# Kernel tuning notes

Measured on AMD Instinct MI355X. Metric: run time of the kernel, lower is better.

## Reference

```python
import jax, jax.numpy as jnp
import numpy as np

TOP_K = 2          # routed top_k = top_k - num_shared_experts = 3 - 1
CAP_FACTOR = 1.1   # capacity_factor


def setup_inputs() -> dict:
    key = jax.random.key(0)
    ks = jax.random.split(key, 12)
    B, S, D, E = 4, 2048, 1024, 7
    s = 0.02
    return {
        "x": jax.random.normal(ks[0], (B, S, D), jnp.float32),
        "noise": jax.random.normal(ks[1], (B, S, E), jnp.float32),
        "Wr": jax.random.normal(ks[2], (D, E)) * s, "br": jnp.zeros((E,)),
        "Wn": jax.random.normal(ks[3], (D, E)) * s, "bn": jnp.zeros((E,)),
        "W1": jax.random.normal(ks[4], (E, D, D)) * s, "b1": jnp.zeros((E, D)),
        "W2": jax.random.normal(ks[5], (E, D, D)) * s, "b2": jnp.zeros((E, D)),
        "Ws1": jax.random.normal(ks[6], (D, D)) * s, "bs1": jnp.zeros((D,)),
        "Ws2": jax.random.normal(ks[7], (D, D)) * s, "bs2": jnp.zeros((D,)),
    }


def reference(x, noise, Wr, br, Wn, bn, W1, b1, W2, b2, Ws1, bs1, Ws2, bs2):
    B, S, D = x.shape
    E = Wr.shape[1]
    N = B * S
    C = int(N * TOP_K / E * CAP_FACTOR)  # per-expert capacity (static)

    # shared expert (Dropout inactive at inference)
    x_shared = jax.nn.relu(x @ Ws1 + bs1) @ Ws2 + bs2

    # --- noisy top-k router ---
    logits = x @ Wr + br
    noisy = logits + noise * jax.nn.softplus(x @ Wn + bn)
    vals, idx = jax.lax.top_k(noisy, TOP_K)                    # [B,S,K]
    onehot = jax.nn.one_hot(idx, E, dtype=x.dtype)             # [B,S,K,E]
    probs_k = jax.nn.softmax(vals, axis=-1)                    # softmax over -inf-masked logits == softmax over top-k vals
    router_probs = jnp.einsum('bske,bsk->bse', onehot, probs_k)
    expert_mask = onehot.sum(-2)
    lbl = E * (router_probs.mean((0, 1)) * expert_mask.mean((0, 1))).sum()

    # --- capacity-limited dispatch, first-come-first-served in flat token order ---
    flat_x = x.reshape(N, D)
    flat_g = router_probs.reshape(N, E)
    m = (expert_mask.reshape(N, E) > 0).T                      # [E,N] token->expert assignment
    pos = jnp.cumsum(m.astype(jnp.int32), axis=1) - 1          # slot within expert
    valid = m & (pos < C)
    token = jnp.arange(N, dtype=jnp.int32)
    dest = jnp.where(valid, jnp.arange(E, dtype=jnp.int32)[:, None] * C + pos, E * C)
    idxs = jnp.full((E * C + 1,), N, dtype=jnp.int32)
    idxs = idxs.at[dest.reshape(-1)].set(jnp.broadcast_to(token, (E, N)).reshape(-1))
    idxs = idxs[:E * C].reshape(E, C)                          # token id per slot, N = padding

    xpad = jnp.concatenate([flat_x, jnp.zeros((1, D), x.dtype)], axis=0)
    gpad = jnp.concatenate([flat_g, jnp.zeros((1, E), x.dtype)], axis=0)
    xe = xpad[idxs]                                            # [E,C,D]
    h = jax.nn.relu(jnp.einsum('ecd,edh->ech', xe, W1) + b1[:, None, :])
    out = jnp.einsum('ech,ehd->ecd', h, W2) + b2[:, None, :]
    g = (gpad[idxs] * jnp.eye(E, dtype=x.dtype)[:, None, :]).sum(-1)  # [E,C] gate per slot
    slot_valid = (idxs < N).astype(x.dtype)
    weighted = out * (g * slot_valid)[..., None]

    upd = jnp.zeros((N + 1, D), x.dtype).at[idxs.reshape(-1)].add(weighted.reshape(-1, D))[:N]
    final = upd.reshape(B, S, D) + x_shared
    return final, lbl
```

## Files before the change

kernel.cpp:

```cpp
#include <hip/hip_runtime.h>
#include <math.h>

typedef unsigned short u16;
typedef __attribute__((ext_vector_type(4))) float f32x4;
typedef __bf16 bf16x8 __attribute__((ext_vector_type(8)));

#define NTOK 8192
#define DDIM 1024
#define NEXP 7
#define CAPC 2574
#define CPAD 2688
#define MBE8 11
#define EB8 (NEXP * MBE8 * 4)
#define TB8 (EB8 + 32 * 4)

__device__ inline float bf2f(u16 u) {
    union { unsigned int i; float f; } c; c.i = ((unsigned int)u) << 16; return c.f;
}
__device__ inline u16 f2bf(float f) {
    union { float f; unsigned int i; } c; c.f = f;
    unsigned int u = c.i;
    unsigned int r = (u + 0x7fffu + ((u >> 16) & 1u)) >> 16;
    return (u16)r;
}

__device__ inline void gl2lds16(const u16* g, const u16* l) {
    __builtin_amdgcn_global_load_lds(
        (const __attribute__((address_space(1))) unsigned int*)g,
        (__attribute__((address_space(3))) unsigned int*)l, 16, 0, 0);
}

#define BAR()    asm volatile("s_barrier" ::: "memory")
#define WAITV0() asm volatile("s_waitcnt vmcnt(0)" ::: "memory")

__global__ void k_zero(float* out, long n) {
    long i = (long)blockIdx.x * 256 + threadIdx.x;
    long stride = (long)gridDim.x * 256;
    for (; i < n; i += stride) out[i] = 0.f;
}

__global__ void k_prep(const float* __restrict__ x, u16* __restrict__ xb,
                       int* __restrict__ slot_token, u16* __restrict__ zrow,
                       const float* __restrict__ W1, const float* __restrict__ Ws1,
                       u16* __restrict__ Wt, u16* __restrict__ Wst,
                       const float* __restrict__ W2, const float* __restrict__ Ws2,
                       u16* __restrict__ Wt2, u16* __restrict__ Wst2) {
    int bid = blockIdx.x, tid = threadIdx.x;
    if (bid < 4096) {
        int gid = bid * 256 + tid;
        int i = gid * 8;
        float4 a = *(const float4*)(x + i);
        float4 b = *(const float4*)(x + i + 4);
        ushort4 o0; o0.x = f2bf(a.x); o0.y = f2bf(a.y); o0.z = f2bf(a.z); o0.w = f2bf(a.w);
        ushort4 o1; o1.x = f2bf(b.x); o1.y = f2bf(b.y); o1.z = f2bf(b.z); o1.w = f2bf(b.w);
        *(ushort4*)(xb + i) = o0;
        *(ushort4*)(xb + i + 4) = o1;
        if (gid < DDIM) zrow[gid] = 0;
        if (gid < NEXP * CPAD + 128) slot_token[gid] = NTOK;
        return;
    }
    int phase2 = (bid >= 8192);
    int tb = bid - (phase2 ? 8192 : 4096);
    const float* srcE = phase2 ? W2 : W1;
    const float* srcS = phase2 ? Ws2 : Ws1;
    u16* dE = phase2 ? Wt2 : Wt;
    u16* dS = phase2 ? Wst2 : Wst;
    int z = tb >> 9; int rem = tb & 511;
    int y = rem >> 2; int xq = rem & 3;
    const float* src; u16* dst;
    if (z < 7) { src = srcE + (long)z * 1048576; dst = dE + (long)z * 1048576; }
    else       { src = srcS;                     dst = dS; }
    int n = xq * 256 + tid;
    int k0 = y * 8;
    u16 v[8];
#pragma unroll
    for (int j = 0; j < 8; ++j) v[j] = f2bf(src[(long)(k0 + j) * 1024 + n]);
    ushort4 a; a.x = v[0]; a.y = v[1]; a.z = v[2]; a.w = v[3];
    ushort4 b; b.x = v[4]; b.y = v[5]; b.z = v[6]; b.w = v[7];
    *(ushort4*)(dst + (long)n * 1024 + k0) = a;
    *(ushort4*)(dst + (long)n * 1024 + k0 + 4) = b;
}

__global__ void k_transpose(const float* __restrict__ srcE, const float* __restrict__ srcS,
                            u16* __restrict__ Wt, u16* __restrict__ Wst) {
    int z = blockIdx.z;
    const float* src; u16* dst;
    if (z < 7) { src = srcE + (long)z * 1048576; dst = Wt + (long)z * 1048576; }
    else       { src = srcS;                     dst = Wst; }
    int n = blockIdx.x * 256 + threadIdx.x;
    int k0 = blockIdx.y * 8;
    u16 v[8];
#pragma unroll
    for (int j = 0; j < 8; ++j) v[j] = f2bf(src[(long)(k0 + j) * 1024 + n]);
    ushort4 a; a.x = v[0]; a.y = v[1]; a.z = v[2]; a.w = v[3];
    ushort4 b; b.x = v[4]; b.y = v[5]; b.z = v[6]; b.w = v[7];
    *(ushort4*)(dst + (long)n * 1024 + k0) = a;
    *(ushort4*)(dst + (long)n * 1024 + k0 + 4) = b;
}

__global__ __launch_bounds__(512) void k_router(
    const float* __restrict__ x,
    const float* __restrict__ Wr, const float* __restrict__ Wn,
    double* __restrict__ arO, double* __restrict__ anO) {
    __shared__ float swr[7168];
    __shared__ float swn[7168];
    int tid = threadIdx.x;
    for (int i = tid; i < 7168; i += 512) { swr[i] = Wr[i]; swn[i] = Wn[i]; }
    __syncthreads();
    int lane = tid & 63, wv = tid >> 6;
    int t = blockIdx.x * 8 + wv;
    double ar[7] = {0,0,0,0,0,0,0}, an[7] = {0,0,0,0,0,0,0};
    for (int j = 0; j < 16; ++j) {
        int d = j * 64 + lane;
        double xd = (double)x[t * 1024 + d];
#pragma unroll
        for (int e = 0; e < 7; ++e) {
            ar[e] += xd * (double)swr[d * 7 + e];
            an[e] += xd * (double)swn[d * 7 + e];
        }
    }
#pragma unroll
    for (int e = 0; e < 7; ++e) {
        for (int o = 32; o > 0; o >>= 1) {
            ar[e] += __shfl_xor(ar[e], o);
            an[e] += __shfl_xor(an[e], o);
        }
    }
    if (lane == 0) {
#pragma unroll
        for (int e = 0; e < 7; ++e) { arO[t * 7 + e] = ar[e]; anO[t * 7 + e] = an[e]; }
    }
}

__global__ void k_tail(const double* __restrict__ arO, const double* __restrict__ anO,
                       const float* __restrict__ noise,
                       const float* __restrict__ br, const float* __restrict__ bn,
                       int* __restrict__ idx0, int* __restrict__ idx1,
                       float* __restrict__ p0, float* __restrict__ p1,
                       int* __restrict__ cntA, double* __restrict__ sumA) {
    int t = blockIdx.x * 256 + threadIdx.x;
    int lane = threadIdx.x & 63;
    double best = -1e300, second = -1e300; int b0 = 0, b1 = 0;
#pragma unroll
    for (int e = 0; e < 7; ++e) {
        double lg = arO[t * 7 + e] + (double)br[e];
        double z  = anO[t * 7 + e] + (double)bn[e];
        double sp = (z > 30.0) ? (z + log1p(exp(-z))) : log1p(exp(z));
        double v  = lg + (double)noise[t * 7 + e] * sp;
        if (v > best)        { second = best; b1 = b0; best = v; b0 = e; }
        else if (v > second) { second = v; b1 = e; }
    }
    double ex = exp(second - best);
    float q0 = (float)(1.0 / (1.0 + ex));
    float q1 = (float)(ex / (1.0 + ex));
    idx0[t] = b0; idx1[t] = b1; p0[t] = q0; p1[t] = q1;
    int chunk = t >> 6;
    double dq0 = (double)q0, dq1 = (double)q1;
#pragma unroll
    for (int e = 0; e < 7; ++e) {
        unsigned long long m = __ballot((b0 == e) || (b1 == e));
        double q = (b0 == e ? dq0 : 0.0) + (b1 == e ? dq1 : 0.0);
        for (int o = 32; o > 0; o >>= 1) q += __shfl_xor(q, o);
        if (lane == 0) { cntA[e * 128 + chunk] = __popcll(m); sumA[e * 128 + chunk] = q; }
    }
}

__global__ void k_scanbase(const int* __restrict__ cntA, const double* __restrict__ sumA,
                           int* __restrict__ baseA, int* __restrict__ cnt,
                           float* __restrict__ out) {
    __shared__ int s[128];
    __shared__ double rd[128];
    __shared__ int rawc[7];
    __shared__ double ps[7];
    int tid = threadIdx.x;
    for (int e = 0; e < 7; ++e) {
        int v = 0;
        if (tid < 128) { v = cntA[e * 128 + tid]; s[tid] = v; }
        if (tid < 128) rd[tid] = sumA[e * 128 + tid];
        __syncthreads();
        for (int o = 1; o < 128; o <<= 1) {
            int add = 0;
            if (tid < 128 && tid >= o) add = s[tid - o];
            __syncthreads();
            if (tid < 128) s[tid] += add;
            __syncthreads();
        }
        if (tid < 128) baseA[e * 128 + tid] = s[tid] - v;
        if (tid == 127) { rawc[e] = s[127]; cnt[e] = (s[127] < CAPC) ? s[127] : CAPC; }
        for (int o = 64; o > 0; o >>= 1) {
            if (tid < o) rd[tid] += rd[tid + o];
            __syncthreads();
        }
        if (tid == 0) ps[e] = rd[0];
        __syncthreads();
    }
    if (tid == 0) {
        double acc = 0.0;
        for (int e = 0; e < 7; ++e) acc += ps[e] * (double)rawc[e];
        out[(long)NTOK * DDIM] = (float)(7.0 * acc / (8192.0 * 8192.0));
    }
}

__global__ void k_assign(const int* __restrict__ idx0, const int* __restrict__ idx1,
                         const int* __restrict__ baseA, int* __restrict__ slot_token,
                         int* __restrict__ ts0, int* __restrict__ ts1) {
    int lane = threadIdx.x & 63;
    int chunk = (blockIdx.x * 256 + threadIdx.x) >> 6;
    int t = chunk * 64 + lane;
    int i0 = idx0[t], i1 = idx1[t];
    int myts0 = -1, myts1 = -1;
    unsigned long long lt = (1ull << lane) - 1ull;
#pragma unroll
    for (int e = 0; e < 7; ++e) {
        bool has = (i0 == e) || (i1 == e);
        unsigned long long m = __ballot(has);
        int pre = __popcll(m & lt);
        int pos = baseA[e * 128 + chunk] + pre;
        if (has && pos < CAPC) {
            int slot = e * CPAD + pos;
            slot_token[slot] = t;
            if (i0 == e) myts0 = slot; else myts1 = slot;
        }
    }
    ts0[t] = myts0; ts1[t] = myts1;
}


#define READ_A(MQ)                                                                      \
    _Pragma("unroll")                                                                   \
    for (int j = 0; j < 4; ++j) {                                                       \
        int row_ = wm * 128 + (MQ) * 64 + j * 16 + rl;                                  \
        _Pragma("unroll")                                                               \
        for (int kh = 0; kh < 2; ++kh)                                                  \
            af[j][kh] = *(const bf16x8*)&sA[row_ * 64 + (((kh * 4 + quad) ^ kq7)) * 8]; \
    }

#define READ_B(NQ)                                                                      \
    _Pragma("unroll")                                                                   \
    for (int j = 0; j < 2; ++j) {                                                       \
        int row_ = wn * 64 + (NQ) * 32 + j * 16 + rl;                                   \
        _Pragma("unroll")                                                               \
        for (int kh = 0; kh < 2; ++kh)                                                  \
            bf[j][kh] = *(const bf16x8*)&sB[row_ * 64 + (((kh * 4 + quad) ^ kq7)) * 8]; \
    }

#define MFMA_Q(MQ, NQ)                                                                  \
    _Pragma("unroll")                                                                   \
    for (int kh = 0; kh < 2; ++kh)                                                      \
        _Pragma("unroll")                                                               \
        for (int j = 0; j < 4; ++j)                                                     \
            _Pragma("unroll")                                                           \
            for (int i = 0; i < 2; ++i)                                                 \
                acc[(MQ) * 4 + j][(NQ) * 2 + i] =                                       \
                    __builtin_amdgcn_mfma_f32_16x16x32_bf16(                            \
                        af[j][kh], bf[i][kh], acc[(MQ) * 4 + j][(NQ) * 2 + i], 0, 0, 0);

template <bool GATHER, bool MODE_H>
__global__ __launch_bounds__(512, 2) void k_gemm8(
    const u16* __restrict__ AbaseE, const u16* __restrict__ AbaseS,
    const int* __restrict__ gidx, const u16* __restrict__ zrow,
    const u16* __restrict__ WtE, const u16* __restrict__ WtS,
    const float* __restrict__ biasE, const float* __restrict__ biasS,
    u16* __restrict__ outE, u16* __restrict__ outS,
    const int* __restrict__ cnt) {
    extern __shared__ __align__(16) u16 lds[];
    int bid = blockIdx.x;
    int tid = threadIdx.x, lane = tid & 63, wv = tid >> 6;
    int lrow = lane >> 3, lkg = lane & 7, kgs = lkg ^ lrow;

    int e = 0, my, nx, mbound;
    const u16* Ab; const u16* Bb; const float* bias; u16* outp;
    bool gather = false;
    if (bid < EB8) {
        e = bid / 44; int r = bid % 44; my = r >> 2; nx = r & 3;
        if (my * 256 >= cnt[e]) return;
        Ab = GATHER ? AbaseE : (AbaseE + (long)e * CPAD * 1024);
        Bb = WtE + ((long)e << 20);
        bias = biasE + e * 1024;
        outp = outE + (long)e * CPAD * 1024;
        gather = GATHER;
        mbound = CPAD;
    } else {
        int sb = bid - EB8; my = sb >> 2; nx = sb & 3;
        Ab = AbaseS; Bb = WtS; bias = biasS; outp = outS;
        mbound = NTOK;
    }
    int m0 = my * 256, n0 = nx * 256;

    const u16* arow[4];
    const u16* brow[4];
#pragma unroll
    for (int i = 0; i < 4; ++i) {
        int r = (wv * 4 + i) * 8 + lrow;
        if (gather) {
            int tok = gidx[e * CPAD + m0 + r];
            arow[i] = (tok < NTOK) ? (AbaseE + (long)tok * DDIM) : zrow;
        } else {
            int rr = m0 + r; if (rr >= mbound) rr = 0;
            arow[i] = Ab + (long)rr * DDIM;
        }
        brow[i] = Bb + (long)(n0 + r) * DDIM;
    }

    f32x4 acc[8][4];
#pragma unroll
    for (int a = 0; a < 8; ++a)
#pragma unroll
        for (int b = 0; b < 4; ++b) { f32x4 z = {0.f, 0.f, 0.f, 0.f}; acc[a][b] = z; }

    int rl = lane & 15, quad = lane >> 4, kq7 = rl & 7;
    int wm = wv >> 2, wn = wv & 3;
    u16* s0 = lds;
    u16* s1 = lds + 32768;

#pragma unroll
    for (int i = 0; i < 4; ++i) {
        gl2lds16(arow[i] + kgs * 8, s0 + (wv * 4 + i) * 512);
        gl2lds16(brow[i] + kgs * 8, s0 + 16384 + (wv * 4 + i) * 512);
    }
    WAITV0();
    BAR();

    bf16x8 af[4][2], bf[2][2];
    for (int T = 0; T < 16; ++T) {
        u16* sc = (T & 1) ? s1 : s0;
        u16* sn = (T & 1) ? s0 : s1;
        const u16* sA = sc;
        const u16* sB = sc + 16384;
        int k1 = (T + 1) * 64;
        READ_A(0)
        READ_B(0)
        if (T < 15) {
#pragma unroll
            for (int i = 0; i < 4; ++i)
                gl2lds16(arow[i] + k1 + kgs * 8, sn + (wv * 4 + i) * 512);
        }
        BAR();
        __builtin_amdgcn_s_setprio(1);
        MFMA_Q(0, 0)
        __builtin_amdgcn_s_setprio(0);
        BAR();
        READ_B(1)
        if (T < 15) {
#pragma unroll
            for (int i = 0; i < 4; ++i)
                gl2lds16(brow[i] + k1 + kgs * 8, sn + 16384 + (wv * 4 + i) * 512);
        }
        BAR();
        __builtin_amdgcn_s_setprio(1);
        MFMA_Q(0, 1)
        __builtin_amdgcn_s_setprio(0);
        BAR();
        READ_A(1)
        BAR();
        __builtin_amdgcn_s_setprio(1);
        MFMA_Q(1, 1)
        __builtin_amdgcn_s_setprio(0);
        BAR();
        READ_B(0)
        BAR();
        __builtin_amdgcn_s_setprio(1);
        MFMA_Q(1, 0)
        __builtin_amdgcn_s_setprio(0);
        WAITV0();
        BAR();
        __builtin_amdgcn_sched_barrier(0);
    }

#pragma unroll
    for (int ni = 0; ni < 4; ++ni) {
        int col = n0 + wn * 64 + ni * 16 + rl;
        float bv = bias[col];
#pragma unroll
        for (int mi = 0; mi < 8; ++mi) {
            int rowb = m0 + wm * 128 + mi * 16 + quad * 4;
#pragma unroll
            for (int r = 0; r < 4; ++r) {
                int rowg = rowb + r;
                if (rowg < mbound) {
                    float v = acc[mi][ni][r] + bv;
                    if constexpr (MODE_H) v = v > 0.f ? v : 0.f;
                    outp[(long)rowg * DDIM + col] = f2bf(v);
                }
            }
        }
    }
}

__global__ __launch_bounds__(256) void k_combine(
    const u16* __restrict__ Xs, const u16* __restrict__ OutE,
    const int* __restrict__ ts0, const int* __restrict__ ts1,
    const float* __restrict__ p0, const float* __restrict__ p1,
    float* __restrict__ out) {
    int b = blockIdx.x;
    int d = threadIdx.x * 4;
    long base = (long)b * DDIM + d;
    ushort4 xs4 = *(const ushort4*)(Xs + base);
    float r0 = bf2f(xs4.x), r1 = bf2f(xs4.y), r2 = bf2f(xs4.z), r3 = bf2f(xs4.w);
    int s0 = ts0[b], s1 = ts1[b];
    if (s0 >= 0) {
        float g = p0[b];
        ushort4 o4 = *(const ushort4*)(OutE + (long)s0 * DDIM + d);
        r0 += g * bf2f(o4.x); r1 += g * bf2f(o4.y); r2 += g * bf2f(o4.z); r3 += g * bf2f(o4.w);
    }
    if (s1 >= 0) {
        float g = p1[b];
        ushort4 o4 = *(const ushort4*)(OutE + (long)s1 * DDIM + d);
        r0 += g * bf2f(o4.x); r1 += g * bf2f(o4.y); r2 += g * bf2f(o4.z); r3 += g * bf2f(o4.w);
    }
    float4 w; w.x = r0; w.y = r1; w.z = r2; w.w = r3;
    *(float4*)(out + base) = w;
}

extern "C" void kernel_launch(void* const* d_in, const int* in_sizes, int n_in,
                              void* d_out, int out_size, void* d_ws, size_t ws_size,
                              hipStream_t stream) {
    const float* x    = (const float*)d_in[0];
    const float* noise= (const float*)d_in[1];
    const float* Wr   = (const float*)d_in[2];
    const float* br   = (const float*)d_in[3];
    const float* Wn   = (const float*)d_in[4];
    const float* bn   = (const float*)d_in[5];
    const float* W1   = (const float*)d_in[6];
    const float* b1   = (const float*)d_in[7];
    const float* W2   = (const float*)d_in[8];
    const float* b2   = (const float*)d_in[9];
    const float* Ws1  = (const float*)d_in[10];
    const float* bs1  = (const float*)d_in[11];
    const float* Ws2  = (const float*)d_in[12];
    const float* bs2  = (const float*)d_in[13];
    float* out = (float*)d_out;
    char* ws = (char*)d_ws;

    size_t off = 0;
    auto alloc = [&](size_t bytes) { size_t o = off; off += (bytes + 255) & ~(size_t)255; return o; };
    u16*  Wt   = (u16*)(ws + alloc(7ull * 1048576 * 2));
    u16*  Wst  = (u16*)(ws + alloc(1048576ull * 2));
    u16*  xb   = (u16*)(ws + alloc((size_t)NTOK * 1024 * 2));
    u16*  He   = (u16*)(ws + alloc((size_t)NEXP * CPAD * 1024 * 2));
    u16*  Hs   = (u16*)(ws + alloc((size_t)NTOK * 1024 * 2));
    u16*  OutE = (u16*)(ws + alloc((size_t)NEXP * CPAD * 1024 * 2));
    u16*  Xs   = (u16*)(ws + alloc((size_t)NTOK * 1024 * 2));
    int*  idx0 = (int*)(ws + alloc(NTOK * 4));
    int*  idx1 = (int*)(ws + alloc(NTOK * 4));
    float* p0  = (float*)(ws + alloc(NTOK * 4));
    float* p1  = (float*)(ws + alloc(NTOK * 4));
    int*  ts0  = (int*)(ws + alloc(NTOK * 4));
    int*  ts1  = (int*)(ws + alloc(NTOK * 4));
    int*  slot_token = (int*)(ws + alloc((NEXP * CPAD + 128) * 4));
    int*  cntA = (int*)(ws + alloc(7 * 128 * 4));
    int*  baseA= (int*)(ws + alloc(7 * 128 * 4));
    double* sumA = (double*)(ws + alloc(7 * 128 * 8));
    int*  cnt    = (int*)(ws + alloc(8 * 4));
    u16*  zrow   = (u16*)(ws + alloc(1024 * 2));
    double* arO  = (double*)(ws + alloc((size_t)NTOK * 7 * 8));
    double* anO  = (double*)(ws + alloc((size_t)NTOK * 7 * 8));
    size_t base_off = off;
    u16*  Wt2  = (u16*)(ws + alloc(7ull * 1048576 * 2));
    u16*  Wst2 = (u16*)(ws + alloc(1048576ull * 2));

    if (base_off > ws_size) {
        k_zero<<<2048, 256, 0, stream>>>(out, (long)out_size);
        return;
    }
    bool sep = (off <= ws_size);
    if (!sep) { Wt2 = Wt; Wst2 = Wst; }

    (void)hipFuncSetAttribute((const void*)k_gemm8<true, true>,
                              hipFuncAttributeMaxDynamicSharedMemorySize, 131072);
    (void)hipFuncSetAttribute((const void*)k_gemm8<false, false>,
                              hipFuncAttributeMaxDynamicSharedMemorySize, 131072);

    k_prep<<<sep ? 12288 : 8192, 256, 0, stream>>>(
        x, xb, slot_token, zrow, W1, Ws1, Wt, Wst, W2, Ws2, Wt2, Wst2);
    k_router<<<1024, 512, 0, stream>>>(x, Wr, Wn, arO, anO);
    k_tail<<<32, 256, 0, stream>>>(arO, anO, noise, br, bn, idx0, idx1, p0, p1, cntA, sumA);
    k_scanbase<<<1, 256, 0, stream>>>(cntA, sumA, baseA, cnt, out);
    k_assign<<<32, 256, 0, stream>>>(idx0, idx1, baseA, slot_token, ts0, ts1);

    k_gemm8<true, true><<<TB8, 512, 131072, stream>>>(
        xb, xb, slot_token, zrow, Wt, Wst, b1, bs1, He, Hs, cnt);

    if (!sep)
        k_transpose<<<dim3(4, 128, 8), 256, 0, stream>>>(W2, Ws2, Wt, Wst);

    k_gemm8<false, false><<<TB8, 512, 131072, stream>>>(
        He, Hs, nullptr, zrow, Wt2, Wst2, b2, bs2, OutE, Xs, cnt);

    k_combine<<<NTOK, 256, 0, stream>>>(Xs, OutE, ts0, ts1, p0, p1, out);
    (void)in_sizes; (void)n_in; (void)out_size;
}
```

Measured before the change: 435.2 us.

## Pipeline GEMM with per-quadrant LDS staging, partial vmcnt waits and XCD-aware block swizzle

Restructures the MoE/shared GEMM main loop into an unrolled two-buffer ping-pong. Each A/B quadrant is staged into LDS separately and earlier than before, and partial vmcnt waits replace full drains, so global loads overlap more of the MFMA work. Block IDs are also remapped so that consecutive logical tiles, which share weight or activation panels, land on the same XCD to improve L2 reuse. The price is more complex buffer reuse logic, where a wrong wait count or overwrite order would race. The 2688 CPAD rows are also read without the old row clamp.

```diff
diff --git a/kernel.cpp b/kernel.cpp
--- a/kernel.cpp
+++ b/kernel.cpp
@@ -10,9 +10,10 @@
 #define NEXP 7
 #define CAPC 2574
 #define CPAD 2688
-#define MBE8 11
-#define EB8 (NEXP * MBE8 * 4)
+#define EB8 (NEXP * 11 * 4)
 #define TB8 (EB8 + 32 * 4)
+#define SWZQ (TB8 / 8)
+#define SWZR (TB8 % 8)
 
 __device__ inline float bf2f(u16 u) {
     union { unsigned int i; float f; } c; c.i = ((unsigned int)u) << 16; return c.f;
@@ -32,6 +33,8 @@
 
 #define BAR()    asm volatile("s_barrier" ::: "memory")
 #define WAITV0() asm volatile("s_waitcnt vmcnt(0)" ::: "memory")
+#define WAITV4() asm volatile("s_waitcnt vmcnt(4)" ::: "memory")
+#define WAITV6() asm volatile("s_waitcnt vmcnt(6)" ::: "memory")
 
 __global__ void k_zero(float* out, long n) {
     long i = (long)blockIdx.x * 256 + threadIdx.x;
@@ -226,25 +229,27 @@
 }
 
 
-#define READ_A(MQ)                                                                      \
+#define RD_AF(DST, MQ, BUF)                                                             \
     _Pragma("unroll")                                                                   \
     for (int j = 0; j < 4; ++j) {                                                       \
         int row_ = wm * 128 + (MQ) * 64 + j * 16 + rl;                                  \
         _Pragma("unroll")                                                               \
         for (int kh = 0; kh < 2; ++kh)                                                  \
-            af[j][kh] = *(const bf16x8*)&sA[row_ * 64 + (((kh * 4 + quad) ^ kq7)) * 8]; \
-    }
-
-#define READ_B(NQ)                                                                      \
+            DST[j][kh] = *(const bf16x8*)&lds[(BUF) + row_ * 64 +                       \
+                                              (((kh * 4 + quad) ^ kq7)) * 8];           \
+    }
+
+#define RD_BF(DST, NQ, BUF)                                                             \
     _Pragma("unroll")                                                                   \
     for (int j = 0; j < 2; ++j) {                                                       \
         int row_ = wn * 64 + (NQ) * 32 + j * 16 + rl;                                   \
         _Pragma("unroll")                                                               \
         for (int kh = 0; kh < 2; ++kh)                                                  \
-            bf[j][kh] = *(const bf16x8*)&sB[row_ * 64 + (((kh * 4 + quad) ^ kq7)) * 8]; \
-    }
-
-#define MFMA_Q(MQ, NQ)                                                                  \
+            DST[j][kh] = *(const bf16x8*)&lds[(BUF) + 16384 + row_ * 64 +               \
+                                              (((kh * 4 + quad) ^ kq7)) * 8];           \
+    }
+
+#define MM(MQ, NQ, AF, BF)                                                              \
     _Pragma("unroll")                                                                   \
     for (int kh = 0; kh < 2; ++kh)                                                      \
         _Pragma("unroll")                                                               \
@@ -253,7 +258,18 @@
             for (int i = 0; i < 2; ++i)                                                 \
                 acc[(MQ) * 4 + j][(NQ) * 2 + i] =                                       \
                     __builtin_amdgcn_mfma_f32_16x16x32_bf16(                            \
-                        af[j][kh], bf[i][kh], acc[(MQ) * 4 + j][(NQ) * 2 + i], 0, 0, 0);
+                        AF[j][kh], BF[i][kh], acc[(MQ) * 4 + j][(NQ) * 2 + i], 0, 0, 0);
+
+#define STG_A(MQ, K, BUF) {                                                             \
+    gl2lds16(pA[MQ][0] + (K) + kgs * 8, lds + (BUF) + dA[MQ][0]);                       \
+    gl2lds16(pA[MQ][1] + (K) + kgs * 8, lds + (BUF) + dA[MQ][1]); }
+
+#define STG_B(NQ, K, BUF) {                                                             \
+    gl2lds16(pB[NQ][0] + (K) + kgs * 8, lds + (BUF) + dB[NQ][0]);                       \
+    gl2lds16(pB[NQ][1] + (K) + kgs * 8, lds + (BUF) + dB[NQ][1]); }
+
+#define PRIO1() __builtin_amdgcn_s_setprio(1)
+#define PRIO0() __builtin_amdgcn_s_setprio(0)
 
 template <bool GATHER, bool MODE_H>
 __global__ __launch_bounds__(512, 2) void k_gemm8(
@@ -264,15 +280,18 @@
     u16* __restrict__ outE, u16* __restrict__ outS,
     const int* __restrict__ cnt) {
     extern __shared__ __align__(16) u16 lds[];
-    int bid = blockIdx.x;
+    int phys = blockIdx.x;
+    int xcd = phys & 7, seq = phys >> 3;
+    int lid = (xcd < SWZR ? xcd * (SWZQ + 1) : SWZR * (SWZQ + 1) + (xcd - SWZR) * SWZQ) + seq;
+
     int tid = threadIdx.x, lane = tid & 63, wv = tid >> 6;
     int lrow = lane >> 3, lkg = lane & 7, kgs = lkg ^ lrow;
 
     int e = 0, my, nx, mbound;
     const u16* Ab; const u16* Bb; const float* bias; u16* outp;
     bool gather = false;
-    if (bid < EB8) {
-        e = bid / 44; int r = bid % 44; my = r >> 2; nx = r & 3;
+    if (lid < EB8) {
+        e = lid / 44; int rr2 = lid % 44; nx = rr2 / 11; my = rr2 % 11;
         if (my * 256 >= cnt[e]) return;
         Ab = GATHER ? AbaseE : (AbaseE + (long)e * CPAD * 1024);
         Bb = WtE + ((long)e << 20);
@@ -281,26 +300,32 @@
         gather = GATHER;
         mbound = CPAD;
     } else {
-        int sb = bid - EB8; my = sb >> 2; nx = sb & 3;
+        int sb = lid - EB8; nx = sb >> 5; my = sb & 31;
         Ab = AbaseS; Bb = WtS; bias = biasS; outp = outS;
         mbound = NTOK;
     }
     int m0 = my * 256, n0 = nx * 256;
 
-    const u16* arow[4];
-    const u16* brow[4];
-#pragma unroll
-    for (int i = 0; i < 4; ++i) {
-        int r = (wv * 4 + i) * 8 + lrow;
-        if (gather) {
-            int tok = gidx[e * CPAD + m0 + r];
-            arow[i] = (tok < NTOK) ? (AbaseE + (long)tok * DDIM) : zrow;
-        } else {
-            int rr = m0 + r; if (rr >= mbound) rr = 0;
-            arow[i] = Ab + (long)rr * DDIM;
-        }
-        brow[i] = Bb + (long)(n0 + r) * DDIM;
-    }
+    const u16* pA[2][2];
+    const u16* pB[2][2];
+    int dA[2][2], dB[2][2];
+#pragma unroll
+    for (int q = 0; q < 2; ++q)
+#pragma unroll
+        for (int j = 0; j < 2; ++j) {
+            int g = wv * 2 + j;
+            int ra = (g >> 3) * 128 + q * 64 + (g & 7) * 8;
+            int rb = (g >> 2) * 64 + q * 32 + (g & 3) * 8;
+            dA[q][j] = ra * 64;
+            dB[q][j] = 16384 + rb * 64;
+            if (gather) {
+                int tok = gidx[e * CPAD + m0 + ra + lrow];
+                pA[q][j] = (tok < NTOK) ? (AbaseE + (long)tok * DDIM) : zrow;
+            } else {
+                pA[q][j] = Ab + (long)(m0 + ra + lrow) * DDIM;
+            }
+            pB[q][j] = Bb + (long)(n0 + rb + lrow) * DDIM;
+        }
 
     f32x4 acc[8][4];
 #pragma unroll
@@ -310,70 +335,51 @@
 
     int rl = lane & 15, quad = lane >> 4, kq7 = rl & 7;
     int wm = wv >> 2, wn = wv & 3;
-    u16* s0 = lds;
-    u16* s1 = lds + 32768;
-
-#pragma unroll
-    for (int i = 0; i < 4; ++i) {
-        gl2lds16(arow[i] + kgs * 8, s0 + (wv * 4 + i) * 512);
-        gl2lds16(brow[i] + kgs * 8, s0 + 16384 + (wv * 4 + i) * 512);
+
+    STG_A(0, 0, 0) STG_B(0, 0, 0) STG_B(1, 0, 0) STG_A(1, 0, 0)
+    STG_A(0, 64, 32768) STG_B(1, 64, 32768) STG_A(1, 64, 32768)
+    WAITV6();
+    BAR();
+
+    bf16x8 afA[4][2], afB[4][2], bfA[2][2], bfB[2][2];
+    for (int t = 0; t < 8; ++t) {
+        int k1 = (2 * t + 1) * 64;
+        int t2 = 2 * t + 2; int k2 = (t2 < 16 ? t2 : 0) * 64;
+        int t3 = 2 * t + 3; int k3 = (t3 < 16 ? t3 : 0) * 64;
+        RD_AF(afA, 0, 0) RD_BF(bfA, 0, 0)
+        STG_B(0, k1, 32768)
+        BAR(); PRIO1(); MM(0, 0, afA, bfA) PRIO0(); BAR();
+        RD_BF(bfB, 1, 0)
+        STG_A(0, k2, 0)
+        BAR(); PRIO1(); MM(0, 1, afA, bfB) PRIO0(); BAR();
+        RD_AF(afB, 1, 0)
+        STG_B(1, k2, 0)
+        BAR(); PRIO1(); MM(1, 1, afB, bfB) PRIO0(); BAR();
+        RD_BF(bfA, 0, 0)
+        STG_A(1, k2, 0)
+        BAR(); PRIO1(); MM(1, 0, afB, bfA) PRIO0(); WAITV4(); BAR();
+        RD_AF(afA, 0, 32768) RD_BF(bfA, 0, 32768)
+        STG_B(0, k2, 0)
+        BAR(); PRIO1(); MM(0, 0, afA, bfA) PRIO0(); BAR();
+        RD_BF(bfB, 1, 32768)
+        STG_A(0, k3, 32768)
+        BAR(); PRIO1(); MM(0, 1, afA, bfB) PRIO0(); BAR();
+        RD_AF(afB, 1, 32768)
+        STG_B(1, k3, 32768)
+        BAR(); PRIO1(); MM(1, 1, afB, bfB) PRIO0(); BAR();
+        RD_BF(bfA, 0, 32768)
+        STG_A(1, k3, 32768)
+        BAR(); PRIO1(); MM(1, 0, afB, bfA) PRIO0(); WAITV4(); BAR();
     }
     WAITV0();
-    BAR();
-
-    bf16x8 af[4][2], bf[2][2];
-    for (int T = 0; T < 16; ++T) {
-        u16* sc = (T & 1) ? s1 : s0;
-        u16* sn = (T & 1) ? s0 : s1;
-        const u16* sA = sc;
-        const u16* sB = sc + 16384;
-        int k1 = (T + 1) * 64;
-        READ_A(0)
-        READ_B(0)
-        if (T < 15) {
-#pragma unroll
-            for (int i = 0; i < 4; ++i)
-                gl2lds16(arow[i] + k1 + kgs * 8, sn + (wv * 4 + i) * 512);
-        }
-        BAR();
-        __builtin_amdgcn_s_setprio(1);
-        MFMA_Q(0, 0)
-        __builtin_amdgcn_s_setprio(0);
-        BAR();
-        READ_B(1)
-        if (T < 15) {
-#pragma unroll
-            for (int i = 0; i < 4; ++i)
-                gl2lds16(brow[i] + k1 + kgs * 8, sn + 16384 + (wv * 4 + i) * 512);
-        }
-        BAR();
-        __builtin_amdgcn_s_setprio(1);
-        MFMA_Q(0, 1)
-        __builtin_amdgcn_s_setprio(0);
-        BAR();
-        READ_A(1)
-        BAR();
-        __builtin_amdgcn_s_setprio(1);
-        MFMA_Q(1, 1)
-        __builtin_amdgcn_s_setprio(0);
-        BAR();
-        READ_B(0)
-        BAR();
-        __builtin_amdgcn_s_setprio(1);
-        MFMA_Q(1, 0)
-        __builtin_amdgcn_s_setprio(0);
-        WAITV0();
-        BAR();
-        __builtin_amdgcn_sched_barrier(0);
-    }
 
 #pragma unroll
     for (int ni = 0; ni < 4; ++ni) {
-        int col = n0 + wn * 64 + ni * 16 + rl;
+        int col = n0 + wn * 64 + (ni >> 1) * 32 + (ni & 1) * 16 + rl;
         float bv = bias[col];
 #pragma unroll
         for (int mi = 0; mi < 8; ++mi) {
-            int rowb = m0 + wm * 128 + mi * 16 + quad * 4;
+            int rowb = m0 + wm * 128 + (mi >> 2) * 64 + (mi & 3) * 16 + quad * 4;
 #pragma unroll
             for (int r = 0; r < 4; ++r) {
                 int rowg = rowb + r;
```

New measurement: 432.5 us. About the same (-0.6%).
